# Kernel optimization log

Measured on AMD Instinct MI355X. Metric: run time of the kernel, lower is better.

The kernel has to match this reference:

```python
import jax, jax.numpy as jnp
import numpy as np

C = 512
B, W, H = 16, 64, 64
K = 128


def setup_inputs() -> dict:
    key = jax.random.key(0)
    ks = jax.random.split(key, 17)
    s = 0.02
    inp = {
        "x1": jax.random.normal(ks[0], (B, C, W, H), jnp.float32),
        "y1": jax.random.normal(ks[1], (B, K, C), jnp.float32),
        "x2": jax.random.normal(ks[2], (B, C, W, H), jnp.float32),
        "y2": jax.random.normal(ks[3], (B, K, C), jnp.float32),
        # 1x1 conv weights stored as [out, in]
        "wq1": jax.random.normal(ks[4], (C // 4, C), jnp.float32) * s,
        "bq1": jnp.zeros((C // 4,), jnp.float32),
        "wq2": jax.random.normal(ks[5], (C // 4, C), jnp.float32) * s,
        "bq2": jnp.zeros((C // 4,), jnp.float32),
        "wk1": jax.random.normal(ks[6], (C // 2, C), jnp.float32) * s,
        "bk1": jnp.zeros((C // 2,), jnp.float32),
        "wk2": jax.random.normal(ks[7], (C // 2, C), jnp.float32) * s,
        "bk2": jnp.zeros((C // 2,), jnp.float32),
        "wv1": jax.random.normal(ks[8], (C, C), jnp.float32) * s,
        "bv1": jnp.zeros((C,), jnp.float32),
        "wv2": jax.random.normal(ks[9], (C, C), jnp.float32) * s,
        "bv2": jnp.zeros((C,), jnp.float32),
        "scale": jnp.ones((1,), jnp.float32) * 0.5,  # nn.Parameter(zeros) would kill grads; nonzero for testing
    }
    return inp


def reference(x1, y1, x2, y2, wq1, bq1, wq2, bq2, wk1, bk1, wk2, bk2,
              wv1, bv1, wv2, bv2, scale):
    b, c, w, h = x1.shape
    n = w * h
    # 1x1 convs == channel-wise linear maps
    q1 = jnp.einsum('bcwh,dc->bdwh', x1, wq1) + bq1[None, :, None, None]
    q2 = jnp.einsum('bcwh,dc->bdwh', x2, wq2) + bq2[None, :, None, None]
    # concat along channels -> [B, C/2, N] -> [B, N, C/2]
    q = jnp.concatenate([q1, q2], axis=1).reshape(b, c // 2, n).transpose(0, 2, 1)
    k1 = y1 @ wk1.T + bk1  # [B, K, C/2]
    k2 = y2 @ wk2.T + bk2
    v1 = y1 @ wv1.T + bv1  # [B, K, C]
    v2 = y2 @ wv2.T + bv2
    e1 = jnp.einsum('bnd,bkd->bnk', q, k1)  # [B, N, K]
    e2 = jnp.einsum('bnd,bkd->bnk', q, k2)
    attn = jax.nn.softmax(jnp.abs(e1 - e2), axis=-1)
    # out = value^T @ attn^T : [B, C, N]
    o1 = jnp.einsum('bkc,bnk->bcn', v1, attn).reshape(b, c, w, h)
    o2 = jnp.einsum('bkc,bnk->bcn', v2, attn).reshape(b, c, w, h)
    out1 = scale[0] * o1 + x1
    out2 = scale[0] * o2 + x2
    return out1, out2
```

## Files before the change

kernel.cpp:

```cpp
#include <hip/hip_runtime.h>

typedef unsigned short u16;
typedef __attribute__((ext_vector_type(8))) short short8v;
typedef __attribute__((ext_vector_type(4))) float floatx4;

#define B_ 16
#define C_ 512
#define N_ 4096
#define K_ 128

__device__ __forceinline__ float bf2f(u16 u) {
    unsigned int x = ((unsigned int)u) << 16;
    return __builtin_bit_cast(float, x);
}
__device__ __forceinline__ u16 f2bf(float f) {
    unsigned int u = __builtin_bit_cast(unsigned int, f);
    u = u + 0x7FFFu + ((u >> 16) & 1u);
    return (u16)(u >> 16);
}
__device__ __forceinline__ void gload_lds16(const u16* g, u16* l) {
    __builtin_amdgcn_global_load_lds(
        (const __attribute__((address_space(1))) void*)g,
        (__attribute__((address_space(3))) void*)l, 16, 0, 0);
}

__global__ void conv_all(const float* __restrict__ y1, const float* __restrict__ y2,
                         const float* __restrict__ wk1, const float* __restrict__ wk2,
                         const float* __restrict__ wv1, const float* __restrict__ wv2,
                         const float* __restrict__ wq1, const float* __restrict__ wq2,
                         u16* y1b, u16* y2b, u16* wk1b, u16* wk2b, u16* wv1b, u16* wv2b,
                         u16* wq1t, u16* wq2t) {
    int tid = blockIdx.x * 256 + threadIdx.x;
    const int SY = B_ * K_ * C_;
    const int SWK = 256 * 512;
    const int SWV = 512 * 512;
    const int SQ = 128 * 512;
    int base = 2*SY + 2*SWK + 2*SWV;
    if (tid < base) {
        const float* src; u16* dst; int off;
        if (tid < SY)                 { src = y1;  dst = y1b;  off = tid; }
        else if (tid < 2*SY)          { src = y2;  dst = y2b;  off = tid - SY; }
        else if (tid < 2*SY+SWK)      { src = wk1; dst = wk1b; off = tid - 2*SY; }
        else if (tid < 2*SY+2*SWK)    { src = wk2; dst = wk2b; off = tid - 2*SY - SWK; }
        else if (tid < 2*SY+2*SWK+SWV){ src = wv1; dst = wv1b; off = tid - 2*SY - 2*SWK; }
        else                          { src = wv2; dst = wv2b; off = tid - 2*SY - 2*SWK - SWV; }
        dst[off] = f2bf(src[off]);
    } else {
        int e = tid - base;
        const float* s = (e >= SQ) ? wq2 : wq1;
        u16* d = (e >= SQ) ? wq2t : wq1t;
        e &= (SQ - 1);
        int dd = e >> 9;
        int c = e & 511;
        d[c * 128 + dd] = f2bf(s[dd * 512 + c]);
    }
}

__global__ void gemm_gkgv(const u16* __restrict__ y1b, const u16* __restrict__ y2b,
                          const u16* __restrict__ wk1b, const u16* __restrict__ wk2b,
                          const u16* __restrict__ wv1b, const u16* __restrict__ wv2b,
                          const float* __restrict__ bk1, const float* __restrict__ bk2,
                          const float* __restrict__ bv1, const float* __restrict__ bv2,
                          u16* k1b, u16* k2b, u16* vt1, u16* vt2) {
    int l = threadIdx.x;
    int id = blockIdx.x;
    const u16 *A, *Bt; const float* bias; u16* outp;
    int m0, n0, po; bool bias_m;
    if (id < 256) {
        int bx = id & 1, by = (id >> 1) & 3, z = id >> 3;
        int b = z >> 1, which = z & 1;
        A = (which ? y2b : y1b) + (size_t)b * K_ * C_;
        Bt = which ? wk2b : wk1b;
        bias = which ? bk2 : bk1;
        outp = (which ? k2b : k1b) + (size_t)b * K_ * 256;
        m0 = bx * 64; n0 = by * 64; po = 256; bias_m = false;
    } else {
        int id2 = id - 256;
        int bx = id2 & 7, by = (id2 >> 3) & 1, z = id2 >> 4;
        int b = z >> 1, which = z & 1;
        A = which ? wv2b : wv1b;
        Bt = (which ? y2b : y1b) + (size_t)b * K_ * C_;
        bias = which ? bv2 : bv1;
        outp = (which ? vt2 : vt1) + (size_t)b * C_ * K_;
        m0 = bx * 64; n0 = by * 64; po = 128; bias_m = true;
    }
    floatx4 acc[4][4] = {};
    for (int ch = 0; ch < 16; ++ch) {
        int koff = ch * 32 + (l >> 4) * 8;
        short8v a[4], wv[4];
#pragma unroll
        for (int mf = 0; mf < 4; ++mf) a[mf] = *(const short8v*)(A + (size_t)(m0 + mf*16 + (l & 15)) * 512 + koff);
#pragma unroll
        for (int nf = 0; nf < 4; ++nf) wv[nf] = *(const short8v*)(Bt + (size_t)(n0 + nf*16 + (l & 15)) * 512 + koff);
#pragma unroll
        for (int mf = 0; mf < 4; ++mf)
#pragma unroll
            for (int nf = 0; nf < 4; ++nf)
                acc[mf][nf] = __builtin_amdgcn_mfma_f32_16x16x32_bf16(a[mf], wv[nf], acc[mf][nf], 0, 0, 0);
    }
#pragma unroll
    for (int mf = 0; mf < 4; ++mf)
#pragma unroll
        for (int nf = 0; nf < 4; ++nf)
#pragma unroll
            for (int rg = 0; rg < 4; ++rg) {
                int m = m0 + mf*16 + (l >> 4)*4 + rg;
                int n = n0 + nf*16 + (l & 15);
                outp[(size_t)m * po + n] = f2bf(acc[mf][nf][rg] + (bias_m ? bias[m] : bias[n]));
            }
}

__global__ void kd_sub(const u16* __restrict__ k1b, const u16* __restrict__ k2b,
                       u16* kd) {
    int tid = blockIdx.x * 256 + threadIdx.x;
    kd[tid] = f2bf(bf2f(k1b[tid]) - bf2f(k2b[tid]));
}

__global__ void ebd_k(const u16* __restrict__ kd,
                      const float* __restrict__ bq1, const float* __restrict__ bq2,
                      float* ebd) {
    int tid = blockIdx.x * 256 + threadIdx.x;
    const u16* kb = kd + (size_t)tid * 256;
    float s = 0.f;
    for (int d = 0; d < 128; ++d) s += bq1[d] * bf2f(kb[d]);
    for (int d = 0; d < 128; ++d) s += bq2[d] * bf2f(kb[128 + d]);
    ebd[tid] = s;
}

__global__ void gemm_gkk(const u16* __restrict__ kd,
                         const u16* __restrict__ wq1t, const u16* __restrict__ wq2t,
                         u16* kkd1, u16* kkd2) {
    int l = threadIdx.x;
    int z = blockIdx.z; int b = z >> 1; int which = z & 1;
    const u16* A = kd + (size_t)b * K_ * 256 + which * 128;
    const u16* Wt = which ? wq2t : wq1t;
    u16* outp = (which ? kkd2 : kkd1) + (size_t)b * K_ * C_;
    int m0 = blockIdx.x * 64, n0 = blockIdx.y * 64;
    floatx4 acc[4][4] = {};
    for (int ch = 0; ch < 4; ++ch) {
        int koff = ch * 32 + (l >> 4) * 8;
        short8v a[4], wv[4];
#pragma unroll
        for (int mf = 0; mf < 4; ++mf) a[mf] = *(const short8v*)(A + (size_t)(m0 + mf*16 + (l & 15)) * 256 + koff);
#pragma unroll
        for (int nf = 0; nf < 4; ++nf) wv[nf] = *(const short8v*)(Wt + (size_t)(n0 + nf*16 + (l & 15)) * 128 + koff);
#pragma unroll
        for (int mf = 0; mf < 4; ++mf)
#pragma unroll
            for (int nf = 0; nf < 4; ++nf)
                acc[mf][nf] = __builtin_amdgcn_mfma_f32_16x16x32_bf16(a[mf], wv[nf], acc[mf][nf], 0, 0, 0);
    }
#pragma unroll
    for (int mf = 0; mf < 4; ++mf)
#pragma unroll
        for (int nf = 0; nf < 4; ++nf)
#pragma unroll
            for (int rg = 0; rg < 4; ++rg) {
                int m = m0 + mf*16 + (l >> 4)*4 + rg;
                int n = n0 + nf*16 + (l & 15);
                outp[(size_t)m * C_ + n] = f2bf(acc[mf][nf][rg]);
            }
}

__global__ __launch_bounds__(256, 3)
void e_attn(const float* __restrict__ x1, const float* __restrict__ x2,
            const u16* __restrict__ kkd1, const u16* __restrict__ kkd2,
            const float* __restrict__ ebd, u16* __restrict__ attnb) {
    __shared__ u16 smem[24576];
    u16* xT[2]  = { smem,         smem + 4096 };
    u16* kkS[2] = { smem + 8192,  smem + 16384 };

    int id = blockIdx.x;
    int sw = ((id & 7) << 7) | (id >> 3);
    int b = sw >> 6;
    int n0 = (sw & 63) * 64;
    int t = threadIdx.x, w = t >> 6, l = t & 63;

    const float* xs[2] = { x1 + (size_t)b * C_ * N_, x2 + (size_t)b * C_ * N_ };
    const u16* kkp[2] = { kkd1 + (size_t)b * K_ * C_, kkd2 + (size_t)b * K_ * C_ };

    floatx4 ed[8] = {};

    float xA0[8], xA1[8], xB0[8], xB1[8];

    auto SLOADX = [&](int s, float (&v0)[8], float (&v1)[8]) {
        int h = s >> 3, c0 = (s & 7) * 64;
        const float* xp = xs[h] + (size_t)(c0 + w * 16 + (l >> 5) * 8) * N_ + n0 + 2 * (l & 31);
#pragma unroll
        for (int j = 0; j < 8; ++j) {
            float2 f = *(const float2*)(xp + (size_t)j * N_);
            v0[j] = f.x; v1[j] = f.y;
        }
    };
    auto SWRITEX = [&](int buf, float (&v0)[8], float (&v1)[8]) {
        short8v p0, p1;
#pragma unroll
        for (int j = 0; j < 8; ++j) { p0[j] = (short)f2bf(v0[j]); p1[j] = (short)f2bf(v1[j]); }
        u16* xb = xT[buf];
        int row0 = 2 * (l & 31);
        int szz = 8 * ((w * 2 + (l >> 5)) ^ ((l & 31) & 7));
        *(short8v*)&xb[row0 * 64 + szz] = p0;
        *(short8v*)&xb[(row0 + 1) * 64 + szz] = p1;
    };
    auto KLDS = [&](int s, int buf) {
        int h = s >> 3, c0 = (s & 7) * 64;
        const u16* kp = kkp[h] + c0;
#pragma unroll
        for (int i = 0; i < 4; ++i) {
            int gi = i * 256 + t;
            int key = gi >> 3, gp = gi & 7;
            gload_lds16(kp + (size_t)key * 512 + (gp ^ (key & 7)) * 8,
                        &kkS[buf][(i * 256 + w * 64) * 8]);
        }
    };
    auto COMPUTE = [&](int buf) {
        u16* xb = xT[buf]; u16* kb = kkS[buf];
#pragma unroll
        for (int cc = 0; cc < 2; ++cc) {
            int g = cc * 4 + (l >> 4);
            int row = w * 16 + (l & 15);
            short8v a = *(const short8v*)&xb[row * 64 + 8 * (g ^ ((row >> 1) & 7))];
#pragma unroll
            for (int kf = 0; kf < 8; ++kf) {
                int key = kf * 16 + (l & 15);
                short8v bb = *(const short8v*)&kb[key * 64 + 8 * (g ^ (key & 7))];
                ed[kf] = __builtin_amdgcn_mfma_f32_16x16x32_bf16(a, bb, ed[kf], 0, 0, 0);
            }
        }
    };

    SLOADX(0, xA0, xA1); KLDS(0, 0);
    SWRITEX(0, xA0, xA1);
    SLOADX(1, xB0, xB1); KLDS(1, 1);
#pragma unroll
    for (int rr = 0; rr < 8; ++rr) {
        int sA = 2 * rr, sB = 2 * rr + 1;
        __syncthreads();
        if (rr > 0) KLDS(sB, 1);
        COMPUTE(0);
        SWRITEX(1, xB0, xB1);
        if (sA + 2 <= 15) SLOADX(sA + 2, xA0, xA1);
        __syncthreads();
        if (sA + 2 <= 15) KLDS(sA + 2, 0);
        COMPUTE(1);
        if (sB + 1 <= 15) SWRITEX(0, xA0, xA1);
        if (sB + 2 <= 15) SLOADX(sB + 2, xB0, xB1);
    }

    float ebv[8];
#pragma unroll
    for (int kf = 0; kf < 8; ++kf) ebv[kf] = ebd[b * 128 + kf * 16 + (l & 15)];
#pragma unroll
    for (int kf = 0; kf < 8; ++kf)
#pragma unroll
        for (int rg = 0; rg < 4; ++rg)
            ed[kf][rg] = fabsf(ed[kf][rg] + ebv[kf]);

    float m4[4];
#pragma unroll
    for (int rg = 0; rg < 4; ++rg) {
        float m = fmaxf(ed[0][rg], ed[1][rg]);
        m = fmaxf(m, fmaxf(ed[2][rg], ed[3][rg]));
        m = fmaxf(m, fmaxf(ed[4][rg], ed[5][rg]));
        m = fmaxf(m, fmaxf(ed[6][rg], ed[7][rg]));
        m4[rg] = m;
    }
#pragma unroll
    for (int st = 1; st < 16; st <<= 1)
#pragma unroll
        for (int rg = 0; rg < 4; ++rg)
            m4[rg] = fmaxf(m4[rg], __shfl_xor(m4[rg], st));

    float s4[4] = {0.f, 0.f, 0.f, 0.f};
#pragma unroll
    for (int kf = 0; kf < 8; ++kf)
#pragma unroll
        for (int rg = 0; rg < 4; ++rg) {
            float e = __expf(ed[kf][rg] - m4[rg]);
            ed[kf][rg] = e;
            s4[rg] += e;
        }
#pragma unroll
    for (int st = 1; st < 16; st <<= 1)
#pragma unroll
        for (int rg = 0; rg < 4; ++rg)
            s4[rg] += __shfl_xor(s4[rg], st);
#pragma unroll
    for (int rg = 0; rg < 4; ++rg) s4[rg] = 1.0f / s4[rg];

    u16* ap = attnb + ((size_t)(b * N_ + n0)) * 128;
#pragma unroll
    for (int rg = 0; rg < 4; ++rg) {
        int row = w * 16 + (l >> 4) * 4 + rg;
#pragma unroll
        for (int kf = 0; kf < 8; ++kf) {
            int col = kf * 16 + (l & 15);
            ap[(size_t)row * 128 + col] = f2bf(ed[kf][rg] * s4[rg]);
        }
    }
}

__global__ __launch_bounds__(256, 2)
void pv_attn(const float* __restrict__ x1, const float* __restrict__ x2,
             const u16* __restrict__ vt1, const u16* __restrict__ vt2,
             const u16* __restrict__ attnb, const float* __restrict__ scale_p,
             float* __restrict__ out1, float* __restrict__ out2) {
    __shared__ u16 As[128 * 128];

    int id = blockIdx.x;
    int sw = ((id & 7) << 9) | (id >> 3);
    int b = sw >> 8;
    int ct = (sw >> 5) & 7;
    int pt = sw & 31;
    int n0 = pt * 128;
    int cb = ct * 128;
    int oi = cb >> 9;
    int cbl = cb & 511;
    int t = threadIdx.x, w = t >> 6, l = t & 63;

    const float sc = scale_p[0];
    const u16* vt = (oi ? vt2 : vt1) + (size_t)b * C_ * K_;
    const float* xr = (oi ? x2 : x1) + (size_t)b * C_ * N_;
    float* op = (oi ? out2 : out1) + (size_t)b * C_ * N_;

    const u16* ap = attnb + ((size_t)(b * N_ + n0)) * 128;
#pragma unroll
    for (int p = 0; p < 8; ++p) {
        int gi = p * 256 + t;
        int px = gi >> 4, gp = gi & 15;
        gload_lds16(ap + (size_t)px * 128 + (gp ^ (px & 15)) * 8,
                    &As[(p * 256 + w * 64) * 8]);
    }

    short8v vf[2][4];
#pragma unroll
    for (int mf = 0; mf < 2; ++mf)
#pragma unroll
        for (int kc = 0; kc < 4; ++kc)
            vf[mf][kc] = *(const short8v*)(vt + (size_t)(cbl + w * 32 + mf * 16 + (l & 15)) * K_ + kc * 32 + (l >> 4) * 8);

    float rs[2][4][8];
#pragma unroll
    for (int mf = 0; mf < 2; ++mf)
#pragma unroll
        for (int rg = 0; rg < 4; ++rg) {
            const float* rp = xr + (size_t)(cbl + w * 32 + mf * 16 + (l >> 4) * 4 + rg) * N_ + n0 + (l & 15);
#pragma unroll
            for (int nf = 0; nf < 8; ++nf)
                rs[mf][rg][nf] = rp[nf * 16];
        }
    __syncthreads();

    floatx4 o[2][8] = {};
#pragma unroll
    for (int kc = 0; kc < 4; ++kc) {
#pragma unroll
        for (int nf = 0; nf < 8; ++nf) {
            int row = nf * 16 + (l & 15);
            int g = kc * 4 + (l >> 4);
            short8v bb = *(const short8v*)&As[row * 128 + 8 * (g ^ (row & 15))];
#pragma unroll
            for (int mf = 0; mf < 2; ++mf)
                o[mf][nf] = __builtin_amdgcn_mfma_f32_16x16x32_bf16(vf[mf][kc], bb, o[mf][nf], 0, 0, 0);
        }
    }

#pragma unroll
    for (int mf = 0; mf < 2; ++mf)
#pragma unroll
        for (int rg = 0; rg < 4; ++rg) {
            float* wp = op + (size_t)(cbl + w * 32 + mf * 16 + (l >> 4) * 4 + rg) * N_ + n0 + (l & 15);
#pragma unroll
            for (int nf = 0; nf < 8; ++nf)
                wp[nf * 16] = sc * o[mf][nf][rg] + rs[mf][rg][nf];
        }
}

extern "C" void kernel_launch(void* const* d_in, const int* in_sizes, int n_in,
                              void* d_out, int out_size, void* d_ws, size_t ws_size,
                              hipStream_t stream) {
    const float* x1 = (const float*)d_in[0];
    const float* y1 = (const float*)d_in[1];
    const float* x2 = (const float*)d_in[2];
    const float* y2 = (const float*)d_in[3];
    const float* wq1 = (const float*)d_in[4];
    const float* bq1 = (const float*)d_in[5];
    const float* wq2 = (const float*)d_in[6];
    const float* bq2 = (const float*)d_in[7];
    const float* wk1 = (const float*)d_in[8];
    const float* bk1 = (const float*)d_in[9];
    const float* wk2 = (const float*)d_in[10];
    const float* bk2 = (const float*)d_in[11];
    const float* wv1 = (const float*)d_in[12];
    const float* bv1 = (const float*)d_in[13];
    const float* wv2 = (const float*)d_in[14];
    const float* bv2 = (const float*)d_in[15];
    const float* scale = (const float*)d_in[16];

    char* ws = (char*)d_ws;
    u16* y1b  = (u16*)(ws + 0);
    u16* y2b  = (u16*)(ws + 2097152);
    u16* wk1b = (u16*)(ws + 4194304);
    u16* wk2b = (u16*)(ws + 4456448);
    u16* wv1b = (u16*)(ws + 4718592);
    u16* wv2b = (u16*)(ws + 5242880);
    u16* wq1t = (u16*)(ws + 5767168);
    u16* wq2t = (u16*)(ws + 5898240);
    u16* k1b  = (u16*)(ws + 6029312);
    u16* k2b  = (u16*)(ws + 7077888);
    u16* kd   = (u16*)(ws + 8126464);
    u16* kkd1 = (u16*)(ws + 9175040);
    u16* kkd2 = (u16*)(ws + 11272192);
    u16* vt1  = (u16*)(ws + 13369344);
    u16* vt2  = (u16*)(ws + 15466496);
    float* ebd = (float*)(ws + 17563648);
    u16* attnb = (u16*)(ws + 17571840);

    float* out1 = (float*)d_out;
    float* out2 = out1 + (size_t)B_ * C_ * N_;

    hipLaunchKernelGGL(conv_all, dim3(11776), dim3(256), 0, stream,
                       y1, y2, wk1, wk2, wv1, wv2, wq1, wq2,
                       y1b, y2b, wk1b, wk2b, wv1b, wv2b, wq1t, wq2t);
    hipLaunchKernelGGL(gemm_gkgv, dim3(768), dim3(64), 0, stream,
                       y1b, y2b, wk1b, wk2b, wv1b, wv2b, bk1, bk2, bv1, bv2,
                       k1b, k2b, vt1, vt2);
    hipLaunchKernelGGL(kd_sub, dim3(2048), dim3(256), 0, stream, k1b, k2b, kd);
    hipLaunchKernelGGL(ebd_k, dim3(8), dim3(256), 0, stream, kd, bq1, bq2, ebd);
    hipLaunchKernelGGL(gemm_gkk, dim3(2, 8, 32), dim3(64), 0, stream,
                       kd, wq1t, wq2t, kkd1, kkd2);
    hipLaunchKernelGGL(e_attn, dim3(1024), dim3(256), 0, stream,
                       x1, x2, kkd1, kkd2, ebd, attnb);
    hipLaunchKernelGGL(pv_attn, dim3(4096), dim3(256), 0, stream,
                       x1, x2, vt1, vt2, attnb, scale, out1, out2);
}
```

Measured before the change: 246.8 us.

## Fuse score/softmax and PV attention kernels, keeping attn tile in LDS

Merges the e_attn and pv_attn kernels into one fused_attn kernel. Each 512-thread block handles 128 pixels, computes the softmax attention tile, stores it swizzled in LDS, then loops over all 8 output channel chunks to do the PV MFMA and the residual add. This removes the global attn write and read-back and one launch. It also swaps plain syncthreads for explicit vmcnt-waiting barriers. The cost is only 512 blocks, each doing serialized PV work, which lowers parallelism and may cut latency hiding.

```diff
diff --git a/kernel.cpp b/kernel.cpp
--- a/kernel.cpp
+++ b/kernel.cpp
@@ -23,6 +23,12 @@
         (const __attribute__((address_space(1))) void*)g,
         (__attribute__((address_space(3))) void*)l, 16, 0, 0);
 }
+
+#define BARRIER_VM(VMC) do { \
+    asm volatile("s_waitcnt vmcnt(" #VMC ") lgkmcnt(0)" ::: "memory"); \
+    __builtin_amdgcn_s_barrier(); \
+    __builtin_amdgcn_sched_barrier(0); \
+} while (0)
 
 __global__ void conv_all(const float* __restrict__ y1, const float* __restrict__ y2,
                          const float* __restrict__ wk1, const float* __restrict__ wk2,
@@ -162,18 +168,21 @@
             }
 }
 
-__global__ __launch_bounds__(256, 3)
-void e_attn(const float* __restrict__ x1, const float* __restrict__ x2,
-            const u16* __restrict__ kkd1, const u16* __restrict__ kkd2,
-            const float* __restrict__ ebd, u16* __restrict__ attnb) {
-    __shared__ u16 smem[24576];
-    u16* xT[2]  = { smem,         smem + 4096 };
-    u16* kkS[2] = { smem + 8192,  smem + 16384 };
+__global__ __launch_bounds__(512, 4)
+void fused_attn(const float* __restrict__ x1, const float* __restrict__ x2,
+                const u16* __restrict__ kkd1, const u16* __restrict__ kkd2,
+                const u16* __restrict__ vt1, const u16* __restrict__ vt2,
+                const float* __restrict__ ebd, const float* __restrict__ scale_p,
+                float* __restrict__ out1, float* __restrict__ out2) {
+    __shared__ u16 smem[32768];
+    u16* xT[2]  = { smem,         smem + 8192 };
+    u16* kkS[2] = { smem + 16384, smem + 24576 };
+    u16* attn_s = smem + 16384;
 
     int id = blockIdx.x;
-    int sw = ((id & 7) << 7) | (id >> 3);
-    int b = sw >> 6;
-    int n0 = (sw & 63) * 64;
+    int sw = ((id & 7) << 6) | (id >> 3);
+    int b = sw >> 5;
+    int n0 = (sw & 31) * 128;
     int t = threadIdx.x, w = t >> 6, l = t & 63;
 
     const float* xs[2] = { x1 + (size_t)b * C_ * N_, x2 + (size_t)b * C_ * N_ };
@@ -181,36 +190,34 @@
 
     floatx4 ed[8] = {};
 
-    float xA0[8], xA1[8], xB0[8], xB1[8];
-
-    auto SLOADX = [&](int s, float (&v0)[8], float (&v1)[8]) {
+    float xA[16], xB[16];
+
+    auto SLOADX = [&](int s, float (&v)[16]) {
         int h = s >> 3, c0 = (s & 7) * 64;
-        const float* xp = xs[h] + (size_t)(c0 + w * 16 + (l >> 5) * 8) * N_ + n0 + 2 * (l & 31);
-#pragma unroll
-        for (int j = 0; j < 8; ++j) {
-            float2 f = *(const float2*)(xp + (size_t)j * N_);
-            v0[j] = f.x; v1[j] = f.y;
-        }
-    };
-    auto SWRITEX = [&](int buf, float (&v0)[8], float (&v1)[8]) {
+        const float* xp = xs[h] + (size_t)(c0 + (t >> 7) * 16) * N_ + n0 + (t & 127);
+#pragma unroll
+        for (int j = 0; j < 16; ++j) v[j] = xp[(size_t)j * N_];
+    };
+    auto SWRITEX = [&](int buf, float (&v)[16]) {
         short8v p0, p1;
 #pragma unroll
-        for (int j = 0; j < 8; ++j) { p0[j] = (short)f2bf(v0[j]); p1[j] = (short)f2bf(v1[j]); }
+        for (int j = 0; j < 8; ++j) { p0[j] = (short)f2bf(v[j]); p1[j] = (short)f2bf(v[j + 8]); }
         u16* xb = xT[buf];
-        int row0 = 2 * (l & 31);
-        int szz = 8 * ((w * 2 + (l >> 5)) ^ ((l & 31) & 7));
-        *(short8v*)&xb[row0 * 64 + szz] = p0;
-        *(short8v*)&xb[(row0 + 1) * 64 + szz] = p1;
+        int row = t & 127;
+        int g0 = (t >> 7) * 2;
+        int k = (row >> 1) & 7;
+        *(short8v*)&xb[row * 64 + 8 * (g0 ^ k)] = p0;
+        *(short8v*)&xb[row * 64 + 8 * ((g0 + 1) ^ k)] = p1;
     };
     auto KLDS = [&](int s, int buf) {
         int h = s >> 3, c0 = (s & 7) * 64;
         const u16* kp = kkp[h] + c0;
 #pragma unroll
-        for (int i = 0; i < 4; ++i) {
-            int gi = i * 256 + t;
+        for (int i = 0; i < 2; ++i) {
+            int gi = i * 512 + t;
             int key = gi >> 3, gp = gi & 7;
             gload_lds16(kp + (size_t)key * 512 + (gp ^ (key & 7)) * 8,
-                        &kkS[buf][(i * 256 + w * 64) * 8]);
+                        &kkS[buf][(i * 512 + w * 64) * 8]);
         }
     };
     auto COMPUTE = [&](int buf) {
@@ -229,22 +236,23 @@
         }
     };
 
-    SLOADX(0, xA0, xA1); KLDS(0, 0);
-    SWRITEX(0, xA0, xA1);
-    SLOADX(1, xB0, xB1); KLDS(1, 1);
+    SLOADX(0, xA); KLDS(0, 0);
+    SWRITEX(0, xA);
+    SLOADX(1, xB); KLDS(1, 1);
 #pragma unroll
     for (int rr = 0; rr < 8; ++rr) {
         int sA = 2 * rr, sB = 2 * rr + 1;
-        __syncthreads();
+        BARRIER_VM(16);
         if (rr > 0) KLDS(sB, 1);
         COMPUTE(0);
-        SWRITEX(1, xB0, xB1);
-        if (sA + 2 <= 15) SLOADX(sA + 2, xA0, xA1);
-        __syncthreads();
+        SWRITEX(1, xB);
+        if (sA + 2 <= 15) SLOADX(sA + 2, xA);
+        if (rr == 7) { BARRIER_VM(0); }
+        else         { BARRIER_VM(16); }
         if (sA + 2 <= 15) KLDS(sA + 2, 0);
         COMPUTE(1);
-        if (sB + 1 <= 15) SWRITEX(0, xA0, xA1);
-        if (sB + 2 <= 15) SLOADX(sB + 2, xB0, xB1);
+        if (sB + 1 <= 15) SWRITEX(0, xA);
+        if (sB + 2 <= 15) SLOADX(sB + 2, xB);
     }
 
     float ebv[8];
@@ -288,92 +296,70 @@
 #pragma unroll
     for (int rg = 0; rg < 4; ++rg) s4[rg] = 1.0f / s4[rg];
 
-    u16* ap = attnb + ((size_t)(b * N_ + n0)) * 128;
+    __syncthreads();
 #pragma unroll
     for (int rg = 0; rg < 4; ++rg) {
         int row = w * 16 + (l >> 4) * 4 + rg;
 #pragma unroll
         for (int kf = 0; kf < 8; ++kf) {
             int col = kf * 16 + (l & 15);
-            ap[(size_t)row * 128 + col] = f2bf(ed[kf][rg] * s4[rg]);
-        }
-    }
-}
-
-__global__ __launch_bounds__(256, 2)
-void pv_attn(const float* __restrict__ x1, const float* __restrict__ x2,
-             const u16* __restrict__ vt1, const u16* __restrict__ vt2,
-             const u16* __restrict__ attnb, const float* __restrict__ scale_p,
-             float* __restrict__ out1, float* __restrict__ out2) {
-    __shared__ u16 As[128 * 128];
-
-    int id = blockIdx.x;
-    int sw = ((id & 7) << 9) | (id >> 3);
-    int b = sw >> 8;
-    int ct = (sw >> 5) & 7;
-    int pt = sw & 31;
-    int n0 = pt * 128;
-    int cb = ct * 128;
-    int oi = cb >> 9;
-    int cbl = cb & 511;
-    int t = threadIdx.x, w = t >> 6, l = t & 63;
+            attn_s[row * 128 + 8 * ((col >> 3) ^ (row & 15)) + (col & 7)] =
+                f2bf(ed[kf][rg] * s4[rg]);
+        }
+    }
+    __syncthreads();
 
     const float sc = scale_p[0];
-    const u16* vt = (oi ? vt2 : vt1) + (size_t)b * C_ * K_;
-    const float* xr = (oi ? x2 : x1) + (size_t)b * C_ * N_;
-    float* op = (oi ? out2 : out1) + (size_t)b * C_ * N_;
-
-    const u16* ap = attnb + ((size_t)(b * N_ + n0)) * 128;
-#pragma unroll
-    for (int p = 0; p < 8; ++p) {
-        int gi = p * 256 + t;
-        int px = gi >> 4, gp = gi & 15;
-        gload_lds16(ap + (size_t)px * 128 + (gp ^ (px & 15)) * 8,
-                    &As[(p * 256 + w * 64) * 8]);
-    }
-
-    short8v vf[2][4];
-#pragma unroll
-    for (int mf = 0; mf < 2; ++mf)
-#pragma unroll
-        for (int kc = 0; kc < 4; ++kc)
-            vf[mf][kc] = *(const short8v*)(vt + (size_t)(cbl + w * 32 + mf * 16 + (l & 15)) * K_ + kc * 32 + (l >> 4) * 8);
-
-    float rs[2][4][8];
-#pragma unroll
-    for (int mf = 0; mf < 2; ++mf)
+    const u16* vts[2] = { vt1 + (size_t)b * C_ * K_, vt2 + (size_t)b * C_ * K_ };
+    float* outs[2] = { out1 + (size_t)b * C_ * N_, out2 + (size_t)b * C_ * N_ };
+
+    short8v vfA[4], vfB[4];
+    auto LOADVF = [&](int s, short8v (&vf)[4]) {
+        int oi = s >> 2, cc = s & 3;
+        const u16* vp = vts[oi] + (size_t)(cc * 128 + w * 16 + (l & 15)) * K_ + (l >> 4) * 8;
+#pragma unroll
+        for (int kc = 0; kc < 4; ++kc) vf[kc] = *(const short8v*)(vp + kc * 32);
+    };
+    auto COMPPV = [&](int s, short8v (&vf)[4]) {
+        int oi = s >> 2, cc = s & 3;
+        int cr = cc * 128 + w * 16 + (l >> 4) * 4;
+        float rs[4][8];
+        const float* rp = xs[oi] + (size_t)cr * N_ + n0 + (l & 15);
+#pragma unroll
+        for (int rg = 0; rg < 4; ++rg)
+#pragma unroll
+            for (int nf = 0; nf < 8; ++nf)
+                rs[rg][nf] = rp[(size_t)rg * N_ + nf * 16];
+        floatx4 o[8] = {};
+#pragma unroll
+        for (int kc = 0; kc < 4; ++kc) {
+#pragma unroll
+            for (int nf = 0; nf < 8; ++nf) {
+                int row = nf * 16 + (l & 15);
+                int g = kc * 4 + (l >> 4);
+                short8v bb = *(const short8v*)&attn_s[row * 128 + 8 * (g ^ (row & 15))];
+                o[nf] = __builtin_amdgcn_mfma_f32_16x16x32_bf16(vf[kc], bb, o[nf], 0, 0, 0);
+            }
+        }
+        float* op = outs[oi];
 #pragma unroll
         for (int rg = 0; rg < 4; ++rg) {
-            const float* rp = xr + (size_t)(cbl + w * 32 + mf * 16 + (l >> 4) * 4 + rg) * N_ + n0 + (l & 15);
+            size_t rowoff = (size_t)(cr + rg) * N_ + n0 + (l & 15);
 #pragma unroll
             for (int nf = 0; nf < 8; ++nf)
-                rs[mf][rg][nf] = rp[nf * 16];
-        }
-    __syncthreads();
-
-    floatx4 o[2][8] = {};
-#pragma unroll
-    for (int kc = 0; kc < 4; ++kc) {
-#pragma unroll
-        for (int nf = 0; nf < 8; ++nf) {
-            int row = nf * 16 + (l & 15);
-            int g = kc * 4 + (l >> 4);
-            short8v bb = *(const short8v*)&As[row * 128 + 8 * (g ^ (row & 15))];
-#pragma unroll
-            for (int mf = 0; mf < 2; ++mf)
-                o[mf][nf] = __builtin_amdgcn_mfma_f32_16x16x32_bf16(vf[mf][kc], bb, o[mf][nf], 0, 0, 0);
-        }
-    }
-
-#pragma unroll
-    for (int mf = 0; mf < 2; ++mf)
-#pragma unroll
-        for (int rg = 0; rg < 4; ++rg) {
-            float* wp = op + (size_t)(cbl + w * 32 + mf * 16 + (l >> 4) * 4 + rg) * N_ + n0 + (l & 15);
-#pragma unroll
-            for (int nf = 0; nf < 8; ++nf)
-                wp[nf * 16] = sc * o[mf][nf][rg] + rs[mf][rg][nf];
-        }
+                op[rowoff + nf * 16] = sc * o[nf][rg] + rs[rg][nf];
+        }
+    };
+
+    LOADVF(0, vfA);
+    LOADVF(1, vfB);
+#pragma unroll
+    for (int ss = 0; ss < 4; ++ss) {
+        COMPPV(2 * ss, vfA);
+        if (2 * ss + 2 < 8) LOADVF(2 * ss + 2, vfA);
+        COMPPV(2 * ss + 1, vfB);
+        if (2 * ss + 3 < 8) LOADVF(2 * ss + 3, vfB);
+    }
 }
 
 extern "C" void kernel_launch(void* const* d_in, const int* in_sizes, int n_in,
@@ -414,7 +400,6 @@
     u16* vt1  = (u16*)(ws + 13369344);
     u16* vt2  = (u16*)(ws + 15466496);
     float* ebd = (float*)(ws + 17563648);
-    u16* attnb = (u16*)(ws + 17571840);
 
     float* out1 = (float*)d_out;
     float* out2 = out1 + (size_t)B_ * C_ * N_;
@@ -429,8 +414,6 @@
     hipLaunchKernelGGL(ebd_k, dim3(8), dim3(256), 0, stream, kd, bq1, bq2, ebd);
     hipLaunchKernelGGL(gemm_gkk, dim3(2, 8, 32), dim3(64), 0, stream,
                        kd, wq1t, wq2t, kkd1, kkd2);
-    hipLaunchKernelGGL(e_attn, dim3(1024), dim3(256), 0, stream,
-                       x1, x2, kkd1, kkd2, ebd, attnb);
-    hipLaunchKernelGGL(pv_attn, dim3(4096), dim3(256), 0, stream,
-                       x1, x2, vt1, vt2, attnb, scale, out1, out2);
-}
+    hipLaunchKernelGGL(fused_attn, dim3(512), dim3(512), 0, stream,
+                       x1, x2, kkd1, kkd2, vt1, vt2, ebd, scale, out1, out2);
+}
```

Result: faster. 218.5 us (-11.5%).
